# Kernel optimization log

Hardware: AMD Instinct MI355X
Metric: run time of the kernel (lower is better)

## Reference

```python
import jax, jax.numpy as jnp
import numpy as np

B, L, DM = 2, 1024, 768
DI = 2 * DM            # d_inner = 1536
NS = 16                # d_state
DTR = 48               # dt_rank
SCALE = 15             # scale_bits


def _dsp(x):
    # DampenedSquareplus: 0.5 * squareplus(x) = 0.25*(x + sqrt(x^2+4))
    return 0.25 * (x + jnp.sqrt(x * x + 4.0))


def _forward(hidden_states, gamma, W_in, b_in, conv_w, conv_b, W_x, b_x,
             W_dt, b_dt, W_out, b_out, base_decay_nums, res_gate, decay_shifts):
    residual = hidden_states
    # BitShiftNorm: center, then power-of-two RMS scale
    xm = hidden_states - hidden_states.mean(axis=-1, keepdims=True)
    var = (xm * xm).mean(axis=-1, keepdims=True)
    k = jnp.maximum(jnp.round(jnp.log2(jnp.sqrt(var + 1e-9))), 0.0)
    hs = xm * (2.0 ** (-k)) * gamma
    # in_proj (BitLinear modeled as linear)
    xz = hs @ W_in.T + b_in                      # [B,L,2*DI]
    x, z = jnp.split(xz, 2, axis=-1)             # each [B,L,DI]
    # causal depthwise conv1d (kernel 4, left pad 3, truncate to L)
    xt = jnp.transpose(x, (0, 2, 1))             # [B,DI,L]
    xt = jax.lax.conv_general_dilated(
        xt, conv_w, window_strides=(1,), padding=[(3, 0)],
        dimension_numbers=('NCH', 'OIH', 'NCH'), feature_group_count=DI)
    xt = xt + conv_b[None, :, None]
    x = jnp.transpose(xt, (0, 2, 1))             # [B,L,DI]
    x = _dsp(x)
    # x_proj -> dt, B_ssm, C_ssm
    x_dbl = x @ W_x.T + b_x                      # [B,L,DTR+2*NS]
    dt = x_dbl[..., :DTR]
    B_ssm = x_dbl[..., DTR:DTR + NS]
    C_ssm = x_dbl[..., DTR + NS:]
    decay_mod = dt @ W_dt.T + b_dt               # [B,L,DI]
    decay_nums = jnp.clip(base_decay_nums[None, None] + decay_mod[..., None], 0.0, 32767.0)  # [B,L,DI,NS]
    dt_val = _dsp(decay_mod) * 0.1               # [B,L,DI]
    u = (x * dt_val)[..., None] * B_ssm[:, :, None, :]   # [B,L,DI,NS]
    # dyadic decay: a = nums * 2^{-shift}
    a = decay_nums * (2.0 ** (-decay_shifts.astype(jnp.float32)))[None, None]
    F = DI * NS
    u_f = u.reshape(B, L, F)
    a_f = a.reshape(B, L, F)
    # linear recurrence h_t = a_t*h_{t-1} + u_t via associative scan over L
    def combine(c1, c2):
        a1, b1 = c1
        a2, b2 = c2
        return (a1 * a2, a2 * b1 + b2)
    _, h_f = jax.lax.associative_scan(combine, (a_f, u_f), axis=1)
    h_f = jnp.clip(h_f, -32000.0, 32000.0)
    h = h_f.reshape(B, L, DI, NS)
    y = jnp.einsum('bldn,bln->bld', h, C_ssm)    # [B,L,DI]
    # RationalSigmoid gate
    gate = 0.5 * (1.0 + z / jnp.sqrt(z * z + 1.0))
    y = y * gate
    out = y @ W_out.T + b_out
    out = jnp.clip(out, -32000.0, 32000.0)
    return residual + out * res_gate


def setup_inputs() -> dict:
    key = jax.random.key(0)
    ks = jax.random.split(key, 8)
    hidden_states = jax.random.normal(ks[0], (B, L, DM), jnp.float32)
    gamma = jnp.ones((DM,), jnp.float32)
    W_in = jax.random.normal(ks[1], (2 * DI, DM), jnp.float32) / np.float32(np.sqrt(DM))
    b_in = jnp.zeros((2 * DI,), jnp.float32)
    conv_w = jax.random.normal(ks[2], (DI, 1, 4), jnp.float32) * 0.5
    conv_b = jnp.zeros((DI,), jnp.float32)
    W_x = jax.random.normal(ks[3], (DTR + 2 * NS, DI), jnp.float32) / np.float32(np.sqrt(DI))
    b_x = jnp.zeros((DTR + 2 * NS,), jnp.float32)
    W_dt = jax.random.normal(ks[4], (DI, DTR), jnp.float32) * 0.001
    b_dt = jnp.zeros((DI,), jnp.float32)
    W_out = jax.random.normal(ks[5], (DM, DI), jnp.float32) * np.float32(0.02 / np.sqrt(24))
    b_out = jnp.zeros((DM,), jnp.float32)
    # HiPPO-S4D-real-like decays projected to dyadic with shift=15
    n = jnp.arange(NS, dtype=jnp.float32)
    decays = jnp.exp(-0.01 * (n + 1.0))
    base = jnp.round(decays * (2.0 ** SCALE))
    base_decay_nums = jnp.tile(base[None, :], (DI, 1))
    decay_shifts = jnp.full((DI, NS), SCALE, jnp.int32)
    res_gate = jnp.full((1,), 0.5, jnp.float32)  # nonzero so output depends on branch
    return dict(hidden_states=hidden_states, gamma=gamma, W_in=W_in, b_in=b_in,
                conv_w=conv_w, conv_b=conv_b, W_x=W_x, b_x=b_x, W_dt=W_dt, b_dt=b_dt,
                W_out=W_out, b_out=b_out, base_decay_nums=base_decay_nums,
                res_gate=res_gate, decay_shifts=decay_shifts)


def reference(hidden_states, gamma, W_in, b_in, conv_w, conv_b, W_x, b_x,
              W_dt, b_dt, W_out, b_out, base_decay_nums, res_gate, decay_shifts):
    return _forward(hidden_states, gamma, W_in, b_in, conv_w, conv_b, W_x, b_x,
                    W_dt, b_dt, W_out, b_out, base_decay_nums, res_gate, decay_shifts)
```

## Files before the change

### kernel.cpp

```cpp
#include <hip/hip_runtime.h>
#include <hip/hip_bf16.h>
#include <stdint.h>

#define BB  2
#define LL  1024
#define DMM 768
#define DII 1536
#define NSS 16
#define DTRR 48
#define XZN (2*DII)
#define NROWS (BB*LL)
#define N2 1664

#define CHUNKS 64
#define CHLEN  (LL/CHUNKS)
#define NCH    (BB*DII*NSS)

typedef _Float16 h16;
typedef __attribute__((ext_vector_type(8))) _Float16 h16x8;
typedef __attribute__((ext_vector_type(4))) float f32x4;

typedef const __attribute__((address_space(1))) uint32_t gau32;
typedef __attribute__((address_space(3))) uint32_t lau32;
#define GLL16(gp, lp) __builtin_amdgcn_global_load_lds((gau32*)(gp), (lau32*)(lp), 16, 0, 0)

__device__ __forceinline__ float dspf(float x) {
    return 0.25f * (x + sqrtf(x*x + 4.0f));
}
__device__ __forceinline__ float clampf(float x, float lo, float hi) {
    return fminf(fmaxf(x, lo), hi);
}

__global__ __launch_bounds__(256) void k_cvt(const float* __restrict__ in,
                                             h16* __restrict__ out, int n) {
    int i = blockIdx.x * 256 + threadIdx.x;
    if (i < n) out[i] = (h16)in[i];
}

__global__ __launch_bounds__(256) void k_w2(const float* __restrict__ W_x,
                                            const float* __restrict__ b_x,
                                            const float* __restrict__ W_dt,
                                            const float* __restrict__ b_dt,
                                            h16* __restrict__ W2,
                                            float* __restrict__ bias2) {
    int i = blockIdx.x;
    int tid = threadIdx.x;
    if (i < DII) {
        __shared__ float wd[DTRR];
        if (tid < DTRR) wd[tid] = W_dt[i * DTRR + tid];
        __syncthreads();
        for (int j = tid; j < DII; j += 256) {
            float s = 0.f;
            #pragma unroll
            for (int k = 0; k < DTRR; ++k) s = fmaf(wd[k], W_x[(size_t)k * DII + j], s);
            W2[(size_t)i * DII + j] = (h16)s;
        }
        if (tid == 0) {
            float s = b_dt[i];
            for (int k = 0; k < DTRR; ++k) s = fmaf(wd[k], b_x[k], s);
            bias2[i] = s;
        }
    } else if (i < DII + 2 * NSS) {
        int r = i - DII;
        for (int j = tid; j < DII; j += 256)
            W2[(size_t)i * DII + j] = (h16)W_x[(size_t)(DTRR + r) * DII + j];
        if (tid == 0) bias2[i] = b_x[DTRR + r];
    } else {
        for (int j = tid; j < DII; j += 256) W2[(size_t)i * DII + j] = (h16)0.f;
        if (tid == 0) bias2[i] = 0.f;
    }
}

__global__ __launch_bounds__(256) void k_norm(const float* __restrict__ hs,
                                              const float* __restrict__ gamma,
                                              h16* __restrict__ out) {
    int row = blockIdx.x;
    const float* p = hs + (size_t)row * DMM;
    __shared__ float red[256];
    int tid = threadIdx.x;

    float s = 0.f;
    for (int i = tid; i < DMM; i += 256) s += p[i];
    red[tid] = s; __syncthreads();
    for (int off = 128; off > 0; off >>= 1) {
        if (tid < off) red[tid] += red[tid + off];
        __syncthreads();
    }
    float mean = red[0] / (float)DMM;
    __syncthreads();

    float v = 0.f;
    for (int i = tid; i < DMM; i += 256) { float d = p[i] - mean; v += d*d; }
    red[tid] = v; __syncthreads();
    for (int off = 128; off > 0; off >>= 1) {
        if (tid < off) red[tid] += red[tid + off];
        __syncthreads();
    }
    float var = red[0] / (float)DMM;
    float k = rintf(log2f(sqrtf(var + 1e-9f)));
    k = fmaxf(k, 0.f);
    float scale = exp2f(-k);
    for (int i = tid; i < DMM; i += 256)
        out[(size_t)row * DMM + i] = (h16)((p[i] - mean) * scale * gamma[i]);
}

template<int EPI>
__global__ __launch_bounds__(256) void k_gemm64(
    const h16* __restrict__ A, int lda,
    const h16* __restrict__ Bw, int ldb,
    const float* __restrict__ bias,
    float* __restrict__ C, int ldc, int K,
    const float* __restrict__ resid, const float* __restrict__ rgate)
{
    __shared__ __align__(16) h16 As[2][64 * 64];
    __shared__ __align__(16) h16 Bs[2][64 * 64];
    const int tid  = threadIdx.x;
    const int lane = tid & 63;
    const int wv   = tid >> 6;
    const int bm = blockIdx.y * 64, bn = blockIdx.x * 64;
    const int wr = wv >> 1, wc = wv & 1;

    f32x4 acc[2][2] = {};

    const int srow = lane >> 3;
    const int kbl  = ((lane & 7) ^ srow) * 8;
    const int KT = K / 64;

    #pragma unroll
    for (int q = 0; q < 2; ++q) {
        int row = (wv * 2 + q) * 8 + srow;
        GLL16(A  + (size_t)(bm + row) * lda + kbl, &As[0][(wv*2+q)*8*64]);
        GLL16(Bw + (size_t)(bn + row) * ldb + kbl, &Bs[0][(wv*2+q)*8*64]);
    }

    int buf = 0;
    for (int kt = 0; kt < KT; ++kt) {
        if (kt + 1 < KT) {
            int k0 = (kt + 1) * 64;
            #pragma unroll
            for (int q = 0; q < 2; ++q) {
                int row = (wv * 2 + q) * 8 + srow;
                GLL16(A  + (size_t)(bm + row) * lda + k0 + kbl, &As[buf^1][(wv*2+q)*8*64]);
                GLL16(Bw + (size_t)(bn + row) * ldb + k0 + kbl, &Bs[buf^1][(wv*2+q)*8*64]);
            }
            asm volatile("s_waitcnt vmcnt(4)" ::: "memory");
        } else {
            asm volatile("s_waitcnt vmcnt(0)" ::: "memory");
        }
        __syncthreads();

        const int r16 = lane & 15, kq = lane >> 4;
        #pragma unroll
        for (int kk = 0; kk < 2; ++kk) {
            h16x8 af[2], bf[2];
            #pragma unroll
            for (int i = 0; i < 2; ++i) {
                int rowA = wr * 32 + i * 16 + r16;
                af[i] = *(const h16x8*)&As[buf][rowA * 64 + (((kk*4 + kq) ^ (rowA & 7)) << 3)];
            }
            #pragma unroll
            for (int j = 0; j < 2; ++j) {
                int rowB = wc * 32 + j * 16 + r16;
                bf[j] = *(const h16x8*)&Bs[buf][rowB * 64 + (((kk*4 + kq) ^ (rowB & 7)) << 3)];
            }
            #pragma unroll
            for (int i = 0; i < 2; ++i)
                #pragma unroll
                for (int j = 0; j < 2; ++j)
                    acc[i][j] = __builtin_amdgcn_mfma_f32_16x16x32_f16(af[i], bf[j], acc[i][j], 0, 0, 0);
        }
        __syncthreads();
        buf ^= 1;
    }

    const int r4 = (lane >> 4) * 4;
    const int cn = lane & 15;
    float rg = 0.f;
    if (EPI) rg = rgate[0];
    #pragma unroll
    for (int i = 0; i < 2; ++i) {
        #pragma unroll
        for (int j = 0; j < 2; ++j) {
            int col = bn + wc * 32 + j * 16 + cn;
            float bv = bias[col];
            #pragma unroll
            for (int r = 0; r < 4; ++r) {
                int row = bm + wr * 32 + i * 16 + r4 + r;
                float v = acc[i][j][r] + bv;
                if (EPI) {
                    v = clampf(v, -32000.f, 32000.f);
                    v = resid[(size_t)row * ldc + col] + v * rg;
                }
                C[(size_t)row * ldc + col] = v;
            }
        }
    }
}

__global__ __launch_bounds__(256) void k_conv(const float* __restrict__ xz,
                                              const float* __restrict__ cw,
                                              const float* __restrict__ cb,
                                              h16* __restrict__ xacth,
                                              h16* __restrict__ gateh)
{
    int idx = blockIdx.x * 256 + threadIdx.x;
    if (idx >= NROWS * DII) return;
    int c = idx % DII;
    int bl = idx / DII;
    int l = bl % LL;
    int b = bl / LL;
    float acc = cb[c];
    #pragma unroll
    for (int j = 0; j < 4; ++j) {
        int ls = l - 3 + j;
        if (ls >= 0)
            acc = fmaf(xz[(size_t)(b * LL + ls) * XZN + c], cw[c * 4 + j], acc);
    }
    xacth[idx] = (h16)dspf(acc);
    float z = xz[(size_t)bl * XZN + DII + c];
    gateh[idx] = (h16)(0.5f * (1.0f + z * rsqrtf(z * z + 1.0f)));
}

__global__ __launch_bounds__(256) void k_scan_p1(
    const float* __restrict__ dmbc,
    const h16*   __restrict__ xacth,
    const float* __restrict__ basenum,
    const int*   __restrict__ shifts,
    float2* __restrict__ st)
{
    int bc   = blockIdx.x / 6;
    int dblk = blockIdx.x % 6;
    int d    = dblk * 256 + threadIdx.x;
    int b    = bc / CHUNKS;
    int chunk= bc % CHUNKS;

    float base[16], p2[16], h[16], A[16];
    #pragma unroll
    for (int n = 0; n < 16; ++n) {
        base[n] = basenum[d * NSS + n];
        p2[n]   = exp2f(-(float)shifts[d * NSS + n]);
        h[n] = 0.f; A[n] = 1.f;
    }
    int row0 = b * LL + chunk * CHLEN;
    #pragma unroll 2
    for (int l = 0; l < CHLEN; ++l) {
        int row = row0 + l;
        float dm = dmbc[(size_t)row * N2 + d];
        float xv = (float)xacth[(size_t)row * DII + d];
        float common = xv * (dspf(dm) * 0.1f);
        const float4* Bp = (const float4*)(dmbc + (size_t)row * N2 + DII);
        float4 B0 = Bp[0], B1 = Bp[1], B2 = Bp[2], B3 = Bp[3];
        const float Bv[16] = {B0.x,B0.y,B0.z,B0.w, B1.x,B1.y,B1.z,B1.w,
                              B2.x,B2.y,B2.z,B2.w, B3.x,B3.y,B3.z,B3.w};
        #pragma unroll
        for (int n = 0; n < 16; ++n) {
            float a = clampf(base[n] + dm, 0.f, 32767.f) * p2[n];
            h[n] = fmaf(a, h[n], common * Bv[n]);
            A[n] *= a;
        }
    }
    size_t sb = ((size_t)bc * DII + d) * 16;
    #pragma unroll
    for (int n = 0; n < 16; ++n) st[sb + n] = make_float2(A[n], h[n]);
}

__global__ __launch_bounds__(256) void k_scan_p2(float2* __restrict__ st)
{
    int ch = blockIdx.x * 256 + threadIdx.x;
    int b  = ch / (DII * NSS);
    int rem = ch - b * (DII * NSS);
    float hin = 0.f;
    #pragma unroll 4
    for (int c = 0; c < CHUNKS; ++c) {
        size_t idx = ((size_t)(b * CHUNKS + c) * (DII * NSS)) + rem;
        float2 s = st[idx];
        st[idx].x = hin;
        hin = fmaf(s.x, hin, s.y);
    }
}

__global__ __launch_bounds__(256) void k_scan_p3(
    const float* __restrict__ dmbc,
    const h16*   __restrict__ xacth,
    const h16*   __restrict__ gateh,
    const float* __restrict__ basenum,
    const int*   __restrict__ shifts,
    const float2* __restrict__ st,
    h16* __restrict__ ygh)
{
    int bc   = blockIdx.x / 6;
    int dblk = blockIdx.x % 6;
    int d    = dblk * 256 + threadIdx.x;
    int b    = bc / CHUNKS;
    int chunk= bc % CHUNKS;

    float base[16], p2[16], h[16];
    size_t sb = ((size_t)bc * DII + d) * 16;
    #pragma unroll
    for (int n = 0; n < 16; ++n) {
        base[n] = basenum[d * NSS + n];
        p2[n]   = exp2f(-(float)shifts[d * NSS + n]);
        h[n] = st[sb + n].x;
    }
    int row0 = b * LL + chunk * CHLEN;
    #pragma unroll 2
    for (int l = 0; l < CHLEN; ++l) {
        int row = row0 + l;
        float dm = dmbc[(size_t)row * N2 + d];
        float xv = (float)xacth[(size_t)row * DII + d];
        float common = xv * (dspf(dm) * 0.1f);
        const float4* Bp = (const float4*)(dmbc + (size_t)row * N2 + DII);
        float4 B0 = Bp[0], B1 = Bp[1], B2 = Bp[2], B3 = Bp[3];
        float4 C0 = Bp[4], C1 = Bp[5], C2 = Bp[6], C3 = Bp[7];
        const float Bv[16] = {B0.x,B0.y,B0.z,B0.w, B1.x,B1.y,B1.z,B1.w,
                              B2.x,B2.y,B2.z,B2.w, B3.x,B3.y,B3.z,B3.w};
        const float Cv[16] = {C0.x,C0.y,C0.z,C0.w, C1.x,C1.y,C1.z,C1.w,
                              C2.x,C2.y,C2.z,C2.w, C3.x,C3.y,C3.z,C3.w};
        float y = 0.f;
        #pragma unroll
        for (int n = 0; n < 16; ++n) {
            float a = clampf(base[n] + dm, 0.f, 32767.f) * p2[n];
            h[n] = fmaf(a, h[n], common * Bv[n]);
            float hc = clampf(h[n], -32000.f, 32000.f);
            y = fmaf(hc, Cv[n], y);
        }
        float gate = (float)gateh[(size_t)row * DII + d];
        ygh[(size_t)row * DII + d] = (h16)(y * gate);
    }
}

extern "C" void kernel_launch(void* const* d_in, const int* in_sizes, int n_in,
                              void* d_out, int out_size, void* d_ws, size_t ws_size,
                              hipStream_t stream) {
    const float* hs        = (const float*)d_in[0];
    const float* gamma     = (const float*)d_in[1];
    const float* W_in      = (const float*)d_in[2];
    const float* b_in      = (const float*)d_in[3];
    const float* conv_w    = (const float*)d_in[4];
    const float* conv_b    = (const float*)d_in[5];
    const float* W_x       = (const float*)d_in[6];
    const float* b_x       = (const float*)d_in[7];
    const float* W_dt      = (const float*)d_in[8];
    const float* b_dt      = (const float*)d_in[9];
    const float* W_out     = (const float*)d_in[10];
    const float* b_out     = (const float*)d_in[11];
    const float* base_dec  = (const float*)d_in[12];
    const float* res_gate  = (const float*)d_in[13];
    const int*   dec_shift = (const int*)d_in[14];

    char* w = (char*)d_ws;
    float* XZ    = (float*)w;  w += (size_t)NROWS * XZN * 4;
    h16*   XACTH = (h16*)w;    w += (size_t)NROWS * DII * 2;
    float* DMBC  = (float*)w;  w += (size_t)NROWS * N2  * 4;
    h16*   W2H   = (h16*)w;    w += (size_t)N2 * DII * 2;
    h16*   WOH   = (h16*)w;    w += (size_t)DMM * DII * 2;
    float* BIAS2 = (float*)w;  w += 8192;
    h16*   YGH   = (h16*)w;    w += (size_t)NROWS * DII * 2;
    h16*   HSNH  = (h16*)w;    w += (size_t)NROWS * DMM * 2;
    h16*   WINH  = (h16*)w;    w += (size_t)XZN * DMM * 2;
    float2* SCST  = (float2*)XZ;
    h16*    GATEH = HSNH;

    float* out = (float*)d_out;

    k_cvt<<<(XZN * DMM + 255) / 256, 256, 0, stream>>>(W_in, WINH, XZN * DMM);
    k_cvt<<<(DMM * DII + 255) / 256, 256, 0, stream>>>(W_out, WOH, DMM * DII);
    k_w2<<<N2, 256, 0, stream>>>(W_x, b_x, W_dt, b_dt, W2H, BIAS2);

    k_norm<<<NROWS, 256, 0, stream>>>(hs, gamma, HSNH);

    k_gemm64<0><<<dim3(XZN / 64, NROWS / 64), 256, 0, stream>>>(
        HSNH, DMM, WINH, DMM, b_in, XZ, XZN, DMM, nullptr, nullptr);

    k_conv<<<(NROWS * DII) / 256, 256, 0, stream>>>(XZ, conv_w, conv_b, XACTH, GATEH);

    k_gemm64<0><<<dim3(N2 / 64, NROWS / 64), 256, 0, stream>>>(
        XACTH, DII, W2H, DII, BIAS2, DMBC, N2, DII, nullptr, nullptr);

    k_scan_p1<<<BB * CHUNKS * 6, 256, 0, stream>>>(
        DMBC, XACTH, base_dec, dec_shift, SCST);
    k_scan_p2<<<NCH / 256, 256, 0, stream>>>(SCST);
    k_scan_p3<<<BB * CHUNKS * 6, 256, 0, stream>>>(
        DMBC, XACTH, GATEH, base_dec, dec_shift, SCST, YGH);

    k_gemm64<1><<<dim3(DMM / 64, NROWS / 64), 256, 0, stream>>>(
        YGH, DII, WOH, DII, b_out, out, DMM, DII, hs, res_gate);
}
```

Before: 179.8 us.

## Store GEMM intermediates in fp16, fuse gate into scan, swizzle GEMM blocks

The in_proj and x_proj GEMMs now write fp16 outputs instead of fp32, roughly halving the traffic the conv and scan kernels read. The gate activation is no longer stored by the conv kernel; scan phase 3 computes it directly from z. Scan state moves to separate A and H arrays with fewer chunks. GEMM workgroups get an XCD-aware block remap. The risk is lost accuracy from holding decay_mod and the B/C projections in fp16, plus longer sequential work per chunk in the scan.

```diff
diff --git a/kernel.cpp b/kernel.cpp
--- a/kernel.cpp
+++ b/kernel.cpp
@@ -12,7 +12,7 @@
 #define NROWS (BB*LL)
 #define N2 1664
 
-#define CHUNKS 64
+#define CHUNKS 32
 #define CHLEN  (LL/CHUNKS)
 #define NCH    (BB*DII*NSS)
 
@@ -104,12 +104,12 @@
         out[(size_t)row * DMM + i] = (h16)((p[i] - mean) * scale * gamma[i]);
 }
 
-template<int EPI>
+template<int EPI, typename OutT>
 __global__ __launch_bounds__(256) void k_gemm64(
     const h16* __restrict__ A, int lda,
     const h16* __restrict__ Bw, int ldb,
     const float* __restrict__ bias,
-    float* __restrict__ C, int ldc, int K,
+    OutT* __restrict__ C, int ldc, int K,
     const float* __restrict__ resid, const float* __restrict__ rgate)
 {
     __shared__ __align__(16) h16 As[2][64 * 64];
@@ -117,7 +117,14 @@
     const int tid  = threadIdx.x;
     const int lane = tid & 63;
     const int wv   = tid >> 6;
-    const int bm = blockIdx.y * 64, bn = blockIdx.x * 64;
+
+    const int nwg = gridDim.x * gridDim.y;
+    const int bid = blockIdx.y * gridDim.x + blockIdx.x;
+    const int cpx = nwg >> 3;
+    const int swz = (bid & 7) * cpx + (bid >> 3);
+    const int bxi = swz % gridDim.x, byi = swz / gridDim.x;
+
+    const int bm = byi * 64, bn = bxi * 64;
     const int wr = wv >> 1, wc = wv & 1;
 
     f32x4 acc[2][2] = {};
@@ -191,17 +198,16 @@
                     v = clampf(v, -32000.f, 32000.f);
                     v = resid[(size_t)row * ldc + col] + v * rg;
                 }
-                C[(size_t)row * ldc + col] = v;
+                C[(size_t)row * ldc + col] = (OutT)v;
             }
         }
     }
 }
 
-__global__ __launch_bounds__(256) void k_conv(const float* __restrict__ xz,
+__global__ __launch_bounds__(256) void k_conv(const h16* __restrict__ xz,
                                               const float* __restrict__ cw,
                                               const float* __restrict__ cb,
-                                              h16* __restrict__ xacth,
-                                              h16* __restrict__ gateh)
+                                              h16* __restrict__ xacth)
 {
     int idx = blockIdx.x * 256 + threadIdx.x;
     if (idx >= NROWS * DII) return;
@@ -214,19 +220,17 @@
     for (int j = 0; j < 4; ++j) {
         int ls = l - 3 + j;
         if (ls >= 0)
-            acc = fmaf(xz[(size_t)(b * LL + ls) * XZN + c], cw[c * 4 + j], acc);
+            acc = fmaf((float)xz[(size_t)(b * LL + ls) * XZN + c], cw[c * 4 + j], acc);
     }
     xacth[idx] = (h16)dspf(acc);
-    float z = xz[(size_t)bl * XZN + DII + c];
-    gateh[idx] = (h16)(0.5f * (1.0f + z * rsqrtf(z * z + 1.0f)));
 }
 
 __global__ __launch_bounds__(256) void k_scan_p1(
-    const float* __restrict__ dmbc,
-    const h16*   __restrict__ xacth,
+    const h16* __restrict__ dmbc,
+    const h16* __restrict__ xacth,
     const float* __restrict__ basenum,
     const int*   __restrict__ shifts,
-    float2* __restrict__ st)
+    float* __restrict__ stA, float* __restrict__ stH)
 {
     int bc   = blockIdx.x / 6;
     int dblk = blockIdx.x % 6;
@@ -234,37 +238,39 @@
     int b    = bc / CHUNKS;
     int chunk= bc % CHUNKS;
 
-    float base[16], p2[16], h[16], A[16];
+    float base[16], p2c[16], h[16], A[16];
     #pragma unroll
     for (int n = 0; n < 16; ++n) {
         base[n] = basenum[d * NSS + n];
-        p2[n]   = exp2f(-(float)shifts[d * NSS + n]);
+        p2c[n]  = exp2f(-(float)shifts[d * NSS + n]);
         h[n] = 0.f; A[n] = 1.f;
     }
     int row0 = b * LL + chunk * CHLEN;
     #pragma unroll 2
     for (int l = 0; l < CHLEN; ++l) {
         int row = row0 + l;
-        float dm = dmbc[(size_t)row * N2 + d];
+        float dm = (float)dmbc[(size_t)row * N2 + d];
         float xv = (float)xacth[(size_t)row * DII + d];
         float common = xv * (dspf(dm) * 0.1f);
-        const float4* Bp = (const float4*)(dmbc + (size_t)row * N2 + DII);
-        float4 B0 = Bp[0], B1 = Bp[1], B2 = Bp[2], B3 = Bp[3];
-        const float Bv[16] = {B0.x,B0.y,B0.z,B0.w, B1.x,B1.y,B1.z,B1.w,
-                              B2.x,B2.y,B2.z,B2.w, B3.x,B3.y,B3.z,B3.w};
+        const h16x8* Bp = (const h16x8*)(dmbc + (size_t)row * N2 + DII);
+        h16x8 b0 = Bp[0], b1 = Bp[1];
+        float Bv[16];
+        #pragma unroll
+        for (int n = 0; n < 8; ++n) { Bv[n] = (float)b0[n]; Bv[8+n] = (float)b1[n]; }
         #pragma unroll
         for (int n = 0; n < 16; ++n) {
-            float a = clampf(base[n] + dm, 0.f, 32767.f) * p2[n];
+            float a = clampf(base[n] + dm, 0.f, 32767.f) * p2c[n];
             h[n] = fmaf(a, h[n], common * Bv[n]);
             A[n] *= a;
         }
     }
     size_t sb = ((size_t)bc * DII + d) * 16;
     #pragma unroll
-    for (int n = 0; n < 16; ++n) st[sb + n] = make_float2(A[n], h[n]);
-}
-
-__global__ __launch_bounds__(256) void k_scan_p2(float2* __restrict__ st)
+    for (int n = 0; n < 16; ++n) { stA[sb + n] = A[n]; stH[sb + n] = h[n]; }
+}
+
+__global__ __launch_bounds__(256) void k_scan_p2(float* __restrict__ stA,
+                                                 const float* __restrict__ stH)
 {
     int ch = blockIdx.x * 256 + threadIdx.x;
     int b  = ch / (DII * NSS);
@@ -273,19 +279,19 @@
     #pragma unroll 4
     for (int c = 0; c < CHUNKS; ++c) {
         size_t idx = ((size_t)(b * CHUNKS + c) * (DII * NSS)) + rem;
-        float2 s = st[idx];
-        st[idx].x = hin;
-        hin = fmaf(s.x, hin, s.y);
+        float a = stA[idx], hh = stH[idx];
+        stA[idx] = hin;
+        hin = fmaf(a, hin, hh);
     }
 }
 
 __global__ __launch_bounds__(256) void k_scan_p3(
-    const float* __restrict__ dmbc,
-    const h16*   __restrict__ xacth,
-    const h16*   __restrict__ gateh,
+    const h16* __restrict__ dmbc,
+    const h16* __restrict__ xacth,
+    const h16* __restrict__ xz,
     const float* __restrict__ basenum,
     const int*   __restrict__ shifts,
-    const float2* __restrict__ st,
+    const float* __restrict__ stA,
     h16* __restrict__ ygh)
 {
     int bc   = blockIdx.x / 6;
@@ -294,37 +300,39 @@
     int b    = bc / CHUNKS;
     int chunk= bc % CHUNKS;
 
-    float base[16], p2[16], h[16];
+    float base[16], p2c[16], h[16];
     size_t sb = ((size_t)bc * DII + d) * 16;
     #pragma unroll
     for (int n = 0; n < 16; ++n) {
         base[n] = basenum[d * NSS + n];
-        p2[n]   = exp2f(-(float)shifts[d * NSS + n]);
-        h[n] = st[sb + n].x;
+        p2c[n]  = exp2f(-(float)shifts[d * NSS + n]);
+        h[n] = stA[sb + n];
     }
     int row0 = b * LL + chunk * CHLEN;
     #pragma unroll 2
     for (int l = 0; l < CHLEN; ++l) {
         int row = row0 + l;
-        float dm = dmbc[(size_t)row * N2 + d];
+        float dm = (float)dmbc[(size_t)row * N2 + d];
         float xv = (float)xacth[(size_t)row * DII + d];
         float common = xv * (dspf(dm) * 0.1f);
-        const float4* Bp = (const float4*)(dmbc + (size_t)row * N2 + DII);
-        float4 B0 = Bp[0], B1 = Bp[1], B2 = Bp[2], B3 = Bp[3];
-        float4 C0 = Bp[4], C1 = Bp[5], C2 = Bp[6], C3 = Bp[7];
-        const float Bv[16] = {B0.x,B0.y,B0.z,B0.w, B1.x,B1.y,B1.z,B1.w,
-                              B2.x,B2.y,B2.z,B2.w, B3.x,B3.y,B3.z,B3.w};
-        const float Cv[16] = {C0.x,C0.y,C0.z,C0.w, C1.x,C1.y,C1.z,C1.w,
-                              C2.x,C2.y,C2.z,C2.w, C3.x,C3.y,C3.z,C3.w};
+        const h16x8* Bp = (const h16x8*)(dmbc + (size_t)row * N2 + DII);
+        h16x8 b0 = Bp[0], b1 = Bp[1], c0 = Bp[2], c1 = Bp[3];
+        float Bv[16], Cv[16];
+        #pragma unroll
+        for (int n = 0; n < 8; ++n) {
+            Bv[n] = (float)b0[n]; Bv[8+n] = (float)b1[n];
+            Cv[n] = (float)c0[n]; Cv[8+n] = (float)c1[n];
+        }
         float y = 0.f;
         #pragma unroll
         for (int n = 0; n < 16; ++n) {
-            float a = clampf(base[n] + dm, 0.f, 32767.f) * p2[n];
+            float a = clampf(base[n] + dm, 0.f, 32767.f) * p2c[n];
             h[n] = fmaf(a, h[n], common * Bv[n]);
             float hc = clampf(h[n], -32000.f, 32000.f);
             y = fmaf(hc, Cv[n], y);
         }
-        float gate = (float)gateh[(size_t)row * DII + d];
+        float z = (float)xz[(size_t)row * XZN + DII + d];
+        float gate = 0.5f * (1.0f + z * rsqrtf(z * z + 1.0f));
         ygh[(size_t)row * DII + d] = (h16)(y * gate);
     }
 }
@@ -349,17 +357,17 @@
     const int*   dec_shift = (const int*)d_in[14];
 
     char* w = (char*)d_ws;
-    float* XZ    = (float*)w;  w += (size_t)NROWS * XZN * 4;
+    h16*   XZH   = (h16*)w;    w += (size_t)NROWS * XZN * 2;
     h16*   XACTH = (h16*)w;    w += (size_t)NROWS * DII * 2;
-    float* DMBC  = (float*)w;  w += (size_t)NROWS * N2  * 4;
+    h16*   DMBCH = (h16*)w;    w += (size_t)NROWS * N2  * 2;
     h16*   W2H   = (h16*)w;    w += (size_t)N2 * DII * 2;
     h16*   WOH   = (h16*)w;    w += (size_t)DMM * DII * 2;
     float* BIAS2 = (float*)w;  w += 8192;
     h16*   YGH   = (h16*)w;    w += (size_t)NROWS * DII * 2;
     h16*   HSNH  = (h16*)w;    w += (size_t)NROWS * DMM * 2;
     h16*   WINH  = (h16*)w;    w += (size_t)XZN * DMM * 2;
-    float2* SCST  = (float2*)XZ;
-    h16*    GATEH = HSNH;
+    float* STA   = (float*)w;  w += (size_t)BB * CHUNKS * DII * NSS * 4;
+    float* STH   = (float*)w;  w += (size_t)BB * CHUNKS * DII * NSS * 4;
 
     float* out = (float*)d_out;
 
@@ -369,20 +377,20 @@
 
     k_norm<<<NROWS, 256, 0, stream>>>(hs, gamma, HSNH);
 
-    k_gemm64<0><<<dim3(XZN / 64, NROWS / 64), 256, 0, stream>>>(
-        HSNH, DMM, WINH, DMM, b_in, XZ, XZN, DMM, nullptr, nullptr);
-
-    k_conv<<<(NROWS * DII) / 256, 256, 0, stream>>>(XZ, conv_w, conv_b, XACTH, GATEH);
-
-    k_gemm64<0><<<dim3(N2 / 64, NROWS / 64), 256, 0, stream>>>(
-        XACTH, DII, W2H, DII, BIAS2, DMBC, N2, DII, nullptr, nullptr);
+    k_gemm64<0, h16><<<dim3(XZN / 64, NROWS / 64), 256, 0, stream>>>(
+        HSNH, DMM, WINH, DMM, b_in, XZH, XZN, DMM, nullptr, nullptr);
+
+    k_conv<<<(NROWS * DII) / 256, 256, 0, stream>>>(XZH, conv_w, conv_b, XACTH);
+
+    k_gemm64<0, h16><<<dim3(N2 / 64, NROWS / 64), 256, 0, stream>>>(
+        XACTH, DII, W2H, DII, BIAS2, DMBCH, N2, DII, nullptr, nullptr);
 
     k_scan_p1<<<BB * CHUNKS * 6, 256, 0, stream>>>(
-        DMBC, XACTH, base_dec, dec_shift, SCST);
-    k_scan_p2<<<NCH / 256, 256, 0, stream>>>(SCST);
+        DMBCH, XACTH, base_dec, dec_shift, STA, STH);
+    k_scan_p2<<<NCH / 256, 256, 0, stream>>>(STA, STH);
     k_scan_p3<<<BB * CHUNKS * 6, 256, 0, stream>>>(
-        DMBC, XACTH, GATEH, base_dec, dec_shift, SCST, YGH);
-
-    k_gemm64<1><<<dim3(DMM / 64, NROWS / 64), 256, 0, stream>>>(
+        DMBCH, XACTH, XZH, base_dec, dec_shift, STA, YGH);
+
+    k_gemm64<1, float><<<dim3(DMM / 64, NROWS / 64), 256, 0, stream>>>(
         YGH, DII, WOH, DII, b_out, out, DMM, DII, hs, res_gate);
 }
```

New measurement: 186.3 us. 3.6% more time.
